# Performance work log

Hardware: AMD Instinct MI355X
Metric: run time of the kernel (lower is better)

The kernel has to match this reference:

```python
import jax, jax.numpy as jnp
import numpy as np

E, H, I = 5, 768, 1024  # num_experts, hidden_dim, intermediate_dim
TOP_K = 2


def setup_inputs() -> dict:
    key = jax.random.key(0)
    ks = jax.random.split(key, 6)
    s = 0.02
    return {
        "x": jax.random.normal(ks[0], (4, 2048, H), dtype=jnp.float32),
        "router_w": jax.random.normal(ks[1], (E, H), dtype=jnp.float32) * s,  # torch Linear (out,in)
        "router_b": jnp.zeros((E,), dtype=jnp.float32),
        "gate_w": jax.random.normal(ks[2], (E, H, I), dtype=jnp.float32) * s,
        "up_w": jax.random.normal(ks[3], (E, H, I), dtype=jnp.float32) * s,
        "down_w": jax.random.normal(ks[4], (E, I, H), dtype=jnp.float32) * s,
    }


def reference(x, router_w, router_b, gate_w, up_w, down_w):
    B, S, Hd = x.shape
    xf = x.reshape(-1, Hd)                       # [T, H]
    T = xf.shape[0]
    # Router: linear (with bias) -> softmax -> top-2 -> renormalize
    logits = xf @ router_w.T + router_b          # [T, E]
    scores = jax.nn.softmax(logits, axis=-1)
    vals, idx = jax.lax.top_k(scores, TOP_K)     # [T, 2]
    vals = vals / jnp.sum(vals, axis=-1, keepdims=True)
    # Dense combine weights: zero for unselected experts (same math as the
    # per-expert gather/scatter loop in the original module).
    comb = jnp.zeros((T, gate_w.shape[0]), dtype=x.dtype)
    comb = comb.at[jnp.arange(T)[:, None], idx].add(vals)  # [T, E]
    # SwiGLU per expert, vectorized over experts
    g = jnp.einsum('th,ehi->tei', xf, gate_w)    # [T, E, I]
    u = jnp.einsum('th,ehi->tei', xf, up_w)
    y = jnp.einsum('tei,eih->teh', jax.nn.silu(g) * u, down_w)  # [T, E, H]
    out = jnp.einsum('teh,te->th', y, comb)
    return out.reshape(B, S, Hd)
```

## Files before the change

### kernel.cpp

```cpp
#include <hip/hip_runtime.h>
#include <hip/hip_bf16.h>
#include <cstdint>
#include <cstddef>

#define T_TOK 8192
#define H_DIM 768
#define I_DIM 1024
#define N_EXP 5
#define MAXTILE 136

typedef short v8s __attribute__((ext_vector_type(8)));
typedef float v4f __attribute__((ext_vector_type(4)));

static __device__ __forceinline__ unsigned short f2bf(float f) {
    union { float f; unsigned int u; } v; v.f = f;
    unsigned int u = v.u;
    unsigned int r = (u + 0x7fffu + ((u >> 16) & 1u)) >> 16;
    return (unsigned short)r;
}
static __device__ __forceinline__ float bf2f(unsigned short s) {
    union { unsigned int u; float f; } v; v.u = ((unsigned int)s) << 16; return v.f;
}

static __device__ __forceinline__ void async16(const unsigned short* g, unsigned short* l) {
    __builtin_amdgcn_global_load_lds(
        (const __attribute__((address_space(1))) unsigned int*)g,
        (__attribute__((address_space(3))) unsigned int*)l, 16, 0, 0);
}

__global__ void k_prep(const float* __restrict__ gw, const float* __restrict__ uw,
                       const float* __restrict__ dw,
                       unsigned short* __restrict__ wbt, unsigned short* __restrict__ dbt,
                       const float* __restrict__ x, const float* __restrict__ rw,
                       const float* __restrict__ rb, unsigned short* __restrict__ xb,
                       int* __restrict__ top2e, float2* __restrict__ top2w) {
    const int z = blockIdx.z;
    const int tid = threadIdx.x;
    if (z < 3 * N_EXP) {
        __shared__ float tile[32][33];
        const int row = tid >> 3, cq = tid & 7;
        const int ocol = tid >> 3, seg = tid & 7;
        if (z < 2 * N_EXP) {
            if (blockIdx.y >= H_DIM / 32) return;
            const int e = z % N_EXP;
            const int isUp = z >= N_EXP;
            const float* src = (isUp ? uw : gw) + (size_t)e * H_DIM * I_DIM;
            const int c0 = blockIdx.x * 32, r0 = blockIdx.y * 32;
            float4 v = *(const float4*)(src + (size_t)(r0 + row) * I_DIM + c0 + cq * 4);
            tile[row][cq * 4 + 0] = v.x; tile[row][cq * 4 + 1] = v.y;
            tile[row][cq * 4 + 2] = v.z; tile[row][cq * 4 + 3] = v.w;
            __syncthreads();
            int c = c0 + ocol;
            int orow = (c >> 4) * 32 + (c & 15) + (isUp ? 16 : 0);
            ushort4 o;
            o.x = f2bf(tile[seg * 4 + 0][ocol]); o.y = f2bf(tile[seg * 4 + 1][ocol]);
            o.z = f2bf(tile[seg * 4 + 2][ocol]); o.w = f2bf(tile[seg * 4 + 3][ocol]);
            *(ushort4*)(wbt + ((size_t)e * 2 * I_DIM + orow) * H_DIM + r0 + seg * 4) = o;
        } else {
            if (blockIdx.x >= H_DIM / 32) return;
            const int e = z - 2 * N_EXP;
            const float* src = dw + (size_t)e * I_DIM * H_DIM;
            unsigned short* dst = dbt + (size_t)e * I_DIM * H_DIM;
            const int c0 = blockIdx.x * 32, r0 = blockIdx.y * 32;
            float4 v = *(const float4*)(src + (size_t)(r0 + row) * H_DIM + c0 + cq * 4);
            tile[row][cq * 4 + 0] = v.x; tile[row][cq * 4 + 1] = v.y;
            tile[row][cq * 4 + 2] = v.z; tile[row][cq * 4 + 3] = v.w;
            __syncthreads();
            ushort4 o;
            o.x = f2bf(tile[seg * 4 + 0][ocol]); o.y = f2bf(tile[seg * 4 + 1][ocol]);
            o.z = f2bf(tile[seg * 4 + 2][ocol]); o.w = f2bf(tile[seg * 4 + 3][ocol]);
            *(ushort4*)(dst + (size_t)(c0 + ocol) * I_DIM + r0 + seg * 4) = o;
        }
    } else {
        const int wave = tid >> 6, lane = tid & 63;
        const int t = (((z - 3 * N_EXP) * 1024 + blockIdx.y * 32 + blockIdx.x) * 4) + wave;
        const float* xr = x + (size_t)t * H_DIM;
        unsigned short* xbr = xb + (size_t)t * H_DIM;
        float acc[N_EXP];
#pragma unroll
        for (int e = 0; e < N_EXP; e++) acc[e] = 0.f;
#pragma unroll
        for (int j = 0; j < H_DIM / 256; j++) {
            int idx = j * 256 + lane * 4;
            float4 xv = *(const float4*)(xr + idx);
            ushort4 o;
            o.x = f2bf(xv.x); o.y = f2bf(xv.y); o.z = f2bf(xv.z); o.w = f2bf(xv.w);
            *(ushort4*)(xbr + idx) = o;
#pragma unroll
            for (int e = 0; e < N_EXP; e++) {
                float4 wv = *(const float4*)(rw + e * H_DIM + idx);
                acc[e] += xv.x * wv.x + xv.y * wv.y + xv.z * wv.z + xv.w * wv.w;
            }
        }
#pragma unroll
        for (int s = 32; s > 0; s >>= 1) {
#pragma unroll
            for (int e = 0; e < N_EXP; e++) acc[e] += __shfl_down(acc[e], s);
        }
        if (lane == 0) {
            float l[N_EXP];
#pragma unroll
            for (int e = 0; e < N_EXP; e++) l[e] = acc[e] + rb[e];
            int i1 = 0;
#pragma unroll
            for (int e = 1; e < N_EXP; e++) if (l[e] > l[i1]) i1 = e;
            int i2 = (i1 == 0) ? 1 : 0;
#pragma unroll
            for (int e = 0; e < N_EXP; e++) if (e != i1 && l[e] > l[i2]) i2 = e;
            float w1 = 1.f / (1.f + __expf(l[i2] - l[i1]));
            top2e[t] = i1 | (i2 << 8);
            top2w[t] = make_float2(w1, 1.f - w1);
        }
    }
}

__global__ void k_router_b(const int* __restrict__ top2e, const float2* __restrict__ top2w,
                           int* __restrict__ cnt, int* __restrict__ tokslot,
                           float* __restrict__ pweight, int* __restrict__ done,
                           int4* __restrict__ tiles) {
    __shared__ int lcnt[N_EXP], lbase[N_EXP];
    const int tid = threadIdx.x;
    if (tid < N_EXP) lcnt[tid] = 0;
    __syncthreads();
    const int t = blockIdx.x * 256 + tid;
    const int pe = top2e[t];
    const float2 wv = top2w[t];
    const int e1 = pe & 0xff, e2 = pe >> 8;
    const int s1 = atomicAdd(&lcnt[e1], 1);
    const int s2 = atomicAdd(&lcnt[e2], 1);
    __syncthreads();
    if (tid < N_EXP) lbase[tid] = atomicAdd(&cnt[tid], lcnt[tid]);
    __syncthreads();
    const int p1 = lbase[e1] + s1;
    tokslot[e1 * T_TOK + p1] = t; pweight[e1 * T_TOK + p1] = wv.x;
    const int p2 = lbase[e2] + s2;
    tokslot[e2 * T_TOK + p2] = t | (1 << 16); pweight[e2 * T_TOK + p2] = wv.y;
    __syncthreads();
    if (tid == 0) {
        __threadfence();
        if (atomicAdd(done, 1) == (int)gridDim.x - 1) {
            int c[N_EXP], off = 0, idx = 0;
            for (int e = 0; e < N_EXP; e++) c[e] = atomicAdd(&cnt[e], 0);
            for (int e = 0; e < N_EXP; e++) {
                for (int m0 = 0; m0 < c[e]; m0 += 128)
                    tiles[idx++] = make_int4(e, m0, off, c[e]);
                off += c[e];
            }
            for (; idx < MAXTILE; idx++) tiles[idx] = make_int4(-1, 0, 0, 0);
        }
    }
}

__launch_bounds__(256, 4)
__global__ void k_gateup(const unsigned short* __restrict__ xb,
                         const unsigned short* __restrict__ wbt,
                         const int4* __restrict__ tiles,
                         const int* __restrict__ tokslot,
                         const float* __restrict__ pweight,
                         unsigned short* __restrict__ hbuf) {
    const int4 td = tiles[blockIdx.x];
    const int e = td.x;
    if (e < 0) return;
    const int m0 = td.y, offe = td.z, cn = td.w;
    const int n0 = blockIdx.y * 64;

    __shared__ __align__(16) unsigned short ldsA[128 * 64];
    __shared__ __align__(16) unsigned short ldsB[128 * 64];
    __shared__ int tokLds[128];
    __shared__ float pwLds[128];

    const int tid = threadIdx.x;
    if (tid < 128) {
        int gr = m0 + tid;
        int tk = 0; float pw = 0.f;
        if (gr < cn) { tk = tokslot[e * T_TOK + gr] & 0xFFFF; pw = pweight[e * T_TOK + gr]; }
        tokLds[tid] = tk; pwLds[tid] = pw;
    }
    __syncthreads();

    const int lane = tid & 63;
    const int wave = tid >> 6;
    const int fm = lane & 15, quad = lane >> 4;

    const int prow = lane >> 3;
    const int pc = lane & 7;
    const int lc8 = (pc ^ prow) * 8;

    unsigned aOff[4];
#pragma unroll
    for (int c = 0; c < 4; c++)
        aOff[c] = (unsigned)tokLds[c * 32 + wave * 8 + prow] * H_DIM;
    const unsigned short* aBase = xb + lc8;
    const unsigned short* bBase =
        wbt + ((size_t)e * 2 * I_DIM + n0 * 2 + wave * 8 + prow) * H_DIM + lc8;
    unsigned short* ldsAW = ldsA + wave * 8 * 64;
    unsigned short* ldsBW = ldsB + wave * 8 * 64;

    const int wm = (wave & 1) * 64, wnw = wave >> 1;

    v4f acc[4][4];
#pragma unroll
    for (int i = 0; i < 4; i++)
#pragma unroll
        for (int j = 0; j < 4; j++) acc[i][j] = (v4f)0.f;

    for (int kb = 0; kb < H_DIM / 64; kb++) {
        const int k0 = kb * 64;
#pragma unroll
        for (int c = 0; c < 4; c++)
            async16(aBase + aOff[c] + k0, ldsAW + c * 32 * 64);
#pragma unroll
        for (int c = 0; c < 4; c++)
            async16(bBase + (size_t)c * 32 * H_DIM + k0, ldsBW + c * 32 * 64);
        __syncthreads();
#pragma unroll
        for (int ks = 0; ks < 2; ks++) {
            const int pq = ((ks * 4 + quad) ^ (fm & 7)) * 8;
            v8s aF[4], bF[4];
#pragma unroll
            for (int im = 0; im < 4; im++)
                aF[im] = *(const v8s*)&ldsA[(wm + im * 16 + fm) * 64 + pq];
#pragma unroll
            for (int in = 0; in < 4; in++)
                bF[in] = *(const v8s*)&ldsB[(wnw * 64 + in * 16 + fm) * 64 + pq];
#pragma unroll
            for (int im = 0; im < 4; im++)
#pragma unroll
                for (int in = 0; in < 4; in++)
                    acc[im][in] = __builtin_amdgcn_mfma_f32_16x16x32_bf16(aF[im], bF[in], acc[im][in], 0, 0, 0);
        }
        __syncthreads();
    }

#pragma unroll
    for (int im = 0; im < 4; im++) {
#pragma unroll
        for (int reg = 0; reg < 4; reg++) {
            int lr = wm + im * 16 + quad * 4 + reg;
            int gr = m0 + lr;
            if (gr < cn) {
                float pw = pwLds[lr];
                size_t base = (size_t)(offe + gr) * I_DIM + n0 + wnw * 32 + fm;
#pragma unroll
                for (int j = 0; j < 2; j++) {
                    float g = acc[im][2 * j][reg];
                    float u = acc[im][2 * j + 1][reg];
                    float s = g / (1.f + __expf(-g));
                    hbuf[base + j * 16] = f2bf(s * u * pw);
                }
            }
        }
    }
}

__launch_bounds__(256, 4)
__global__ void k_down(const unsigned short* __restrict__ hbuf,
                       const unsigned short* __restrict__ dbt,
                       const int4* __restrict__ tiles,
                       const int* __restrict__ tokslot,
                       unsigned short* __restrict__ ybuf) {
    const int4 td = tiles[blockIdx.x];
    const int e = td.x;
    if (e < 0) return;
    const int m0 = td.y, offe = td.z, cn = td.w;
    const int n0 = blockIdx.y * 128;

    __shared__ __align__(16) unsigned short ldsA[128 * 64];
    __shared__ __align__(16) unsigned short ldsB[128 * 64];
    __shared__ int tokLds[128];

    const int tid = threadIdx.x;
    if (tid < 128) {
        int gr = m0 + tid;
        tokLds[tid] = (gr < cn) ? tokslot[e * T_TOK + gr] : 0;
    }
    __syncthreads();

    const int lane = tid & 63;
    const int wave = tid >> 6;
    const int fm = lane & 15, quad = lane >> 4;

    const int prow = lane >> 3;
    const int pc = lane & 7;
    const int lc8 = (pc ^ prow) * 8;

    unsigned aOff[4];
#pragma unroll
    for (int c = 0; c < 4; c++) {
        int ar = m0 + c * 32 + wave * 8 + prow;
        if (ar >= cn) ar = cn - 1;
        aOff[c] = (unsigned)(offe + ar) * I_DIM;
    }
    const unsigned short* aBase = hbuf + lc8;
    const unsigned short* bBase =
        dbt + ((size_t)e * H_DIM + n0 + wave * 8 + prow) * I_DIM + lc8;
    unsigned short* ldsAW = ldsA + wave * 8 * 64;
    unsigned short* ldsBW = ldsB + wave * 8 * 64;

    const int wm = (wave & 1) * 64, wn = (wave >> 1) * 64;

    v4f acc[4][4];
#pragma unroll
    for (int i = 0; i < 4; i++)
#pragma unroll
        for (int j = 0; j < 4; j++) acc[i][j] = (v4f)0.f;

    for (int kb = 0; kb < I_DIM / 64; kb++) {
        const int k0 = kb * 64;
#pragma unroll
        for (int c = 0; c < 4; c++)
            async16(aBase + aOff[c] + k0, ldsAW + c * 32 * 64);
#pragma unroll
        for (int c = 0; c < 4; c++)
            async16(bBase + (size_t)c * 32 * I_DIM + k0, ldsBW + c * 32 * 64);
        __syncthreads();
#pragma unroll
        for (int ks = 0; ks < 2; ks++) {
            const int pq = ((ks * 4 + quad) ^ (fm & 7)) * 8;
            v8s aF[4], bF[4];
#pragma unroll
            for (int im = 0; im < 4; im++)
                aF[im] = *(const v8s*)&ldsA[(wm + im * 16 + fm) * 64 + pq];
#pragma unroll
            for (int in = 0; in < 4; in++)
                bF[in] = *(const v8s*)&ldsB[(wn + in * 16 + fm) * 64 + pq];
#pragma unroll
            for (int im = 0; im < 4; im++)
#pragma unroll
                for (int in = 0; in < 4; in++)
                    acc[im][in] = __builtin_amdgcn_mfma_f32_16x16x32_bf16(aF[im], bF[in], acc[im][in], 0, 0, 0);
        }
        __syncthreads();
    }

#pragma unroll
    for (int im = 0; im < 4; im++) {
#pragma unroll
        for (int reg = 0; reg < 4; reg++) {
            int lr = wm + im * 16 + quad * 4 + reg;
            int gr = m0 + lr;
            if (gr < cn) {
                int v = tokLds[lr];
                int tok = v & 0xFFFF, s = (v >> 16) & 1;
#pragma unroll
                for (int in = 0; in < 4; in++) {
                    int col = n0 + wn + in * 16 + fm;
                    ybuf[((size_t)s * T_TOK + tok) * H_DIM + col] = f2bf(acc[im][in][reg]);
                }
            }
        }
    }
}

__global__ void k_combine(const unsigned short* __restrict__ ybuf, float* __restrict__ out) {
    const size_t i8 = ((size_t)blockIdx.x * 256 + threadIdx.x) * 8;
    const unsigned short* y0 = ybuf + i8;
    const unsigned short* y1 = ybuf + (size_t)T_TOK * H_DIM + i8;
    ushort4 a0 = *(const ushort4*)y0, a1 = *(const ushort4*)(y0 + 4);
    ushort4 b0 = *(const ushort4*)y1, b1 = *(const ushort4*)(y1 + 4);
    float4 o0, o1;
    o0.x = bf2f(a0.x) + bf2f(b0.x); o0.y = bf2f(a0.y) + bf2f(b0.y);
    o0.z = bf2f(a0.z) + bf2f(b0.z); o0.w = bf2f(a0.w) + bf2f(b0.w);
    o1.x = bf2f(a1.x) + bf2f(b1.x); o1.y = bf2f(a1.y) + bf2f(b1.y);
    o1.z = bf2f(a1.z) + bf2f(b1.z); o1.w = bf2f(a1.w) + bf2f(b1.w);
    *(float4*)(out + i8) = o0;
    *(float4*)(out + i8 + 4) = o1;
}

extern "C" void kernel_launch(void* const* d_in, const int* in_sizes, int n_in,
                              void* d_out, int out_size, void* d_ws, size_t ws_size,
                              hipStream_t stream) {
    const float* x  = (const float*)d_in[0];
    const float* rw = (const float*)d_in[1];
    const float* rb = (const float*)d_in[2];
    const float* gw = (const float*)d_in[3];
    const float* uw = (const float*)d_in[4];
    const float* dw = (const float*)d_in[5];
    float* out = (float*)d_out;

    char* ws = (char*)d_ws;
    size_t o = 0;
    auto alloc = [&](size_t bytes) { void* p = ws + o; o += (bytes + 255) & ~255ull; return p; };
    int*    cnt     = (int*)   alloc(8 * 4);
    int*    tokslot = (int*)   alloc((size_t)N_EXP * T_TOK * 4);
    float*  pweight = (float*) alloc((size_t)N_EXP * T_TOK * 4);
    int*    top2e   = (int*)   alloc((size_t)T_TOK * 4);
    float2* top2w   = (float2*)alloc((size_t)T_TOK * 8);
    int4*   tiles   = (int4*)  alloc((size_t)MAXTILE * 16);
    unsigned short* xb   = (unsigned short*)alloc((size_t)T_TOK * H_DIM * 2);
    unsigned short* wbt  = (unsigned short*)alloc((size_t)N_EXP * 2 * I_DIM * H_DIM * 2);
    unsigned short* dbt  = (unsigned short*)alloc((size_t)N_EXP * H_DIM * I_DIM * 2);
    unsigned short* hbuf = (unsigned short*)alloc((size_t)(2 * T_TOK + 128) * I_DIM * 2);
    unsigned short* ybuf = (unsigned short*)alloc((size_t)2 * T_TOK * H_DIM * 2);

    hipMemsetAsync(cnt, 0, 8 * 4, stream);

    dim3 pg(I_DIM / 32, I_DIM / 32, 3 * N_EXP + 2);
    k_prep<<<pg, 256, 0, stream>>>(gw, uw, dw, wbt, dbt, x, rw, rb, xb, top2e, top2w);

    k_router_b<<<T_TOK / 256, 256, 0, stream>>>(top2e, top2w, cnt, tokslot, pweight,
                                                cnt + 5, tiles);

    dim3 g1(MAXTILE, I_DIM / 64);
    k_gateup<<<g1, 256, 0, stream>>>(xb, wbt, tiles, tokslot, pweight, hbuf);

    dim3 g2(MAXTILE, H_DIM / 128);
    k_down<<<g2, 256, 0, stream>>>(hbuf, dbt, tiles, tokslot, ybuf);

    k_combine<<<(T_TOK * H_DIM) / (256 * 8), 256, 0, stream>>>(ybuf, out);
}
```

Baseline: 232.9 us.

## Rewrite gate/up GEMM as 256x256 tile with double-buffered ping-pong pipeline

The gate/up expert GEMM now uses 512-thread blocks covering 256 tokens by 256 interleaved gate/up columns, with its own 256-row tile list built in the router kernel. The K loop is restructured into a double-buffered LDS pipeline where async global-to-LDS loads for later k-steps are issued between MFMA phases, gated by explicit vmcnt waits, barriers and s_setprio. The goal is to hide load latency and raise data reuse per block. In exchange it uses far more LDS and registers per block, lowers occupancy, and leaves more padded work in each expert's last partial tile.

```diff
diff --git a/kernel.cpp b/kernel.cpp
--- a/kernel.cpp
+++ b/kernel.cpp
@@ -8,6 +8,7 @@
 #define I_DIM 1024
 #define N_EXP 5
 #define MAXTILE 136
+#define MAXT2 72
 
 typedef short v8s __attribute__((ext_vector_type(8)));
 typedef float v4f __attribute__((ext_vector_type(4)));
@@ -117,7 +118,7 @@
 __global__ void k_router_b(const int* __restrict__ top2e, const float2* __restrict__ top2w,
                            int* __restrict__ cnt, int* __restrict__ tokslot,
                            float* __restrict__ pweight, int* __restrict__ done,
-                           int4* __restrict__ tiles) {
+                           int4* __restrict__ tiles, int4* __restrict__ tiles2) {
     __shared__ int lcnt[N_EXP], lbase[N_EXP];
     const int tid = threadIdx.x;
     if (tid < N_EXP) lcnt[tid] = 0;
@@ -147,30 +148,37 @@
                 off += c[e];
             }
             for (; idx < MAXTILE; idx++) tiles[idx] = make_int4(-1, 0, 0, 0);
-        }
-    }
-}
-
-__launch_bounds__(256, 4)
+            int off2 = 0, idx2 = 0;
+            for (int e = 0; e < N_EXP; e++) {
+                for (int m0 = 0; m0 < c[e]; m0 += 256)
+                    tiles2[idx2++] = make_int4(e, m0, off2, c[e]);
+                off2 += c[e];
+            }
+            for (; idx2 < MAXT2; idx2++) tiles2[idx2] = make_int4(-1, 0, 0, 0);
+        }
+    }
+}
+
+__launch_bounds__(512, 2)
 __global__ void k_gateup(const unsigned short* __restrict__ xb,
                          const unsigned short* __restrict__ wbt,
-                         const int4* __restrict__ tiles,
+                         const int4* __restrict__ tiles2,
                          const int* __restrict__ tokslot,
                          const float* __restrict__ pweight,
                          unsigned short* __restrict__ hbuf) {
-    const int4 td = tiles[blockIdx.x];
+    const int4 td = tiles2[blockIdx.y];
     const int e = td.x;
     if (e < 0) return;
     const int m0 = td.y, offe = td.z, cn = td.w;
-    const int n0 = blockIdx.y * 64;
-
-    __shared__ __align__(16) unsigned short ldsA[128 * 64];
-    __shared__ __align__(16) unsigned short ldsB[128 * 64];
-    __shared__ int tokLds[128];
-    __shared__ float pwLds[128];
+    const int by = blockIdx.x;
+
+    __shared__ __align__(16) unsigned short ldsA[2][256 * 64];
+    __shared__ __align__(16) unsigned short ldsB[2][256 * 64];
+    __shared__ int tokLds[256];
+    __shared__ float pwLds[256];
 
     const int tid = threadIdx.x;
-    if (tid < 128) {
+    if (tid < 256) {
         int gr = m0 + tid;
         int tk = 0; float pw = 0.f;
         if (gr < cn) { tk = tokslot[e * T_TOK + gr] & 0xFFFF; pw = pweight[e * T_TOK + gr]; }
@@ -179,68 +187,161 @@
     __syncthreads();
 
     const int lane = tid & 63;
-    const int wave = tid >> 6;
+    const int w = tid >> 6;
     const int fm = lane & 15, quad = lane >> 4;
+    const int wm = (w >> 2) * 128;
+    const int wn = w & 3;
 
     const int prow = lane >> 3;
     const int pc = lane & 7;
     const int lc8 = (pc ^ prow) * 8;
 
-    unsigned aOff[4];
-#pragma unroll
-    for (int c = 0; c < 4; c++)
-        aOff[c] = (unsigned)tokLds[c * 32 + wave * 8 + prow] * H_DIM;
+    unsigned aOff[2][2];
+#pragma unroll
+    for (int h = 0; h < 2; h++)
+#pragma unroll
+        for (int c = 0; c < 2; c++)
+            aOff[h][c] = (unsigned)tokLds[h * 128 + w * 16 + c * 8 + prow] * H_DIM;
     const unsigned short* aBase = xb + lc8;
     const unsigned short* bBase =
-        wbt + ((size_t)e * 2 * I_DIM + n0 * 2 + wave * 8 + prow) * H_DIM + lc8;
-    unsigned short* ldsAW = ldsA + wave * 8 * 64;
-    unsigned short* ldsBW = ldsB + wave * 8 * 64;
-
-    const int wm = (wave & 1) * 64, wnw = wave >> 1;
-
-    v4f acc[4][4];
-#pragma unroll
-    for (int i = 0; i < 4; i++)
+        wbt + ((size_t)e * 2 * I_DIM + by * 256 + w * 16 + prow) * H_DIM + lc8;
+
+#define STAGE_A(buf, h, kt) do { \
+        async16(aBase + aOff[h][0] + (kt) * 64, &ldsA[buf][((h) * 128 + w * 16 + 0) * 64]); \
+        async16(aBase + aOff[h][1] + (kt) * 64, &ldsA[buf][((h) * 128 + w * 16 + 8) * 64]); \
+    } while (0)
+#define STAGE_B(buf, h, kt) do { \
+        async16(bBase + (size_t)((h) * 128 + 0) * H_DIM + (kt) * 64, &ldsB[buf][((h) * 128 + w * 16 + 0) * 64]); \
+        async16(bBase + (size_t)((h) * 128 + 8) * H_DIM + (kt) * 64, &ldsB[buf][((h) * 128 + w * 16 + 8) * 64]); \
+    } while (0)
+
+    v4f acc[8][4];
+#pragma unroll
+    for (int i = 0; i < 8; i++)
 #pragma unroll
         for (int j = 0; j < 4; j++) acc[i][j] = (v4f)0.f;
 
-    for (int kb = 0; kb < H_DIM / 64; kb++) {
-        const int k0 = kb * 64;
-#pragma unroll
-        for (int c = 0; c < 4; c++)
-            async16(aBase + aOff[c] + k0, ldsAW + c * 32 * 64);
-#pragma unroll
-        for (int c = 0; c < 4; c++)
-            async16(bBase + (size_t)c * 32 * H_DIM + k0, ldsBW + c * 32 * 64);
-        __syncthreads();
-#pragma unroll
-        for (int ks = 0; ks < 2; ks++) {
-            const int pq = ((ks * 4 + quad) ^ (fm & 7)) * 8;
-            v8s aF[4], bF[4];
-#pragma unroll
-            for (int im = 0; im < 4; im++)
-                aF[im] = *(const v8s*)&ldsA[(wm + im * 16 + fm) * 64 + pq];
-#pragma unroll
-            for (int in = 0; in < 4; in++)
-                bF[in] = *(const v8s*)&ldsB[(wnw * 64 + in * 16 + fm) * 64 + pq];
-#pragma unroll
-            for (int im = 0; im < 4; im++)
-#pragma unroll
-                for (int in = 0; in < 4; in++)
-                    acc[im][in] = __builtin_amdgcn_mfma_f32_16x16x32_bf16(aF[im], bF[in], acc[im][in], 0, 0, 0);
-        }
-        __syncthreads();
-    }
-
-#pragma unroll
-    for (int im = 0; im < 4; im++) {
+    STAGE_A(0, 0, 0); STAGE_A(0, 1, 0); STAGE_B(0, 0, 0); STAGE_B(0, 1, 0);
+    STAGE_A(1, 0, 1); STAGE_A(1, 1, 1); STAGE_B(1, 0, 1);
+    __builtin_amdgcn_sched_barrier(0);
+    asm volatile("s_waitcnt vmcnt(6)" ::: "memory");
+    __builtin_amdgcn_s_barrier();
+    __builtin_amdgcn_sched_barrier(0);
+
+#pragma unroll 2
+    for (int t = 0; t < H_DIM / 64; t++) {
+        const int cur = t & 1;
+        const unsigned short* A = ldsA[cur];
+        const unsigned short* Bm = ldsB[cur];
+        v8s a03[4][2], a47[4][2], b01[2][2], b23[2][2];
+
+#pragma unroll
+        for (int im = 0; im < 4; im++)
+#pragma unroll
+            for (int ks = 0; ks < 2; ks++)
+                a03[im][ks] = *(const v8s*)&A[(wm + im * 16 + fm) * 64 + (((ks * 4 + quad) ^ (fm & 7)) * 8)];
+#pragma unroll
+        for (int in = 0; in < 2; in++)
+#pragma unroll
+            for (int ks = 0; ks < 2; ks++)
+                b01[in][ks] = *(const v8s*)&Bm[(wn * 64 + in * 16 + fm) * 64 + (((ks * 4 + quad) ^ (fm & 7)) * 8)];
+        if (t + 1 < H_DIM / 64) STAGE_B(cur ^ 1, 1, t + 1);
+        __builtin_amdgcn_sched_barrier(0);
+        __builtin_amdgcn_s_barrier();
+        __builtin_amdgcn_sched_barrier(0);
+        __builtin_amdgcn_s_setprio(1);
+#pragma unroll
+        for (int im = 0; im < 4; im++)
+#pragma unroll
+            for (int in = 0; in < 2; in++)
+#pragma unroll
+                for (int ks = 0; ks < 2; ks++)
+                    acc[im][in] = __builtin_amdgcn_mfma_f32_16x16x32_bf16(a03[im][ks], b01[in][ks], acc[im][in], 0, 0, 0);
+        __builtin_amdgcn_s_setprio(0);
+        __builtin_amdgcn_sched_barrier(0);
+        __builtin_amdgcn_s_barrier();
+        __builtin_amdgcn_sched_barrier(0);
+
+#pragma unroll
+        for (int im = 0; im < 4; im++)
+#pragma unroll
+            for (int ks = 0; ks < 2; ks++)
+                a47[im][ks] = *(const v8s*)&A[(wm + (im + 4) * 16 + fm) * 64 + (((ks * 4 + quad) ^ (fm & 7)) * 8)];
+        __builtin_amdgcn_sched_barrier(0);
+        __builtin_amdgcn_s_barrier();
+        __builtin_amdgcn_sched_barrier(0);
+        __builtin_amdgcn_s_setprio(1);
+#pragma unroll
+        for (int im = 0; im < 4; im++)
+#pragma unroll
+            for (int in = 0; in < 2; in++)
+#pragma unroll
+                for (int ks = 0; ks < 2; ks++)
+                    acc[im + 4][in] = __builtin_amdgcn_mfma_f32_16x16x32_bf16(a47[im][ks], b01[in][ks], acc[im + 4][in], 0, 0, 0);
+        __builtin_amdgcn_s_setprio(0);
+        __builtin_amdgcn_sched_barrier(0);
+        __builtin_amdgcn_s_barrier();
+        __builtin_amdgcn_sched_barrier(0);
+
+#pragma unroll
+        for (int in = 0; in < 2; in++)
+#pragma unroll
+            for (int ks = 0; ks < 2; ks++)
+                b23[in][ks] = *(const v8s*)&Bm[(wn * 64 + (in + 2) * 16 + fm) * 64 + (((ks * 4 + quad) ^ (fm & 7)) * 8)];
+        if (t + 2 < H_DIM / 64) { STAGE_A(cur, 0, t + 2); STAGE_A(cur, 1, t + 2); }
+        __builtin_amdgcn_sched_barrier(0);
+        __builtin_amdgcn_s_barrier();
+        __builtin_amdgcn_sched_barrier(0);
+        __builtin_amdgcn_s_setprio(1);
+#pragma unroll
+        for (int im = 0; im < 4; im++)
+#pragma unroll
+            for (int in = 0; in < 2; in++)
+#pragma unroll
+                for (int ks = 0; ks < 2; ks++)
+                    acc[im][in + 2] = __builtin_amdgcn_mfma_f32_16x16x32_bf16(a03[im][ks], b23[in][ks], acc[im][in + 2], 0, 0, 0);
+        __builtin_amdgcn_s_setprio(0);
+        __builtin_amdgcn_sched_barrier(0);
+        __builtin_amdgcn_s_barrier();
+        __builtin_amdgcn_sched_barrier(0);
+
+        if (t + 2 < H_DIM / 64) STAGE_B(cur, 0, t + 2);
+        __builtin_amdgcn_sched_barrier(0);
+        __builtin_amdgcn_s_barrier();
+        __builtin_amdgcn_sched_barrier(0);
+        __builtin_amdgcn_s_setprio(1);
+#pragma unroll
+        for (int im = 0; im < 4; im++)
+#pragma unroll
+            for (int in = 0; in < 2; in++)
+#pragma unroll
+                for (int ks = 0; ks < 2; ks++)
+                    acc[im + 4][in + 2] = __builtin_amdgcn_mfma_f32_16x16x32_bf16(a47[im][ks], b23[in][ks], acc[im + 4][in + 2], 0, 0, 0);
+        __builtin_amdgcn_s_setprio(0);
+        __builtin_amdgcn_sched_barrier(0);
+
+        if (t < H_DIM / 64 - 2) {
+            asm volatile("s_waitcnt vmcnt(6)" ::: "memory");
+            __builtin_amdgcn_s_barrier();
+            __builtin_amdgcn_sched_barrier(0);
+        } else if (t == H_DIM / 64 - 2) {
+            asm volatile("s_waitcnt vmcnt(0)" ::: "memory");
+            __builtin_amdgcn_s_barrier();
+            __builtin_amdgcn_sched_barrier(0);
+        }
+    }
+#undef STAGE_A
+#undef STAGE_B
+
+#pragma unroll
+    for (int im = 0; im < 8; im++) {
 #pragma unroll
         for (int reg = 0; reg < 4; reg++) {
             int lr = wm + im * 16 + quad * 4 + reg;
             int gr = m0 + lr;
             if (gr < cn) {
                 float pw = pwLds[lr];
-                size_t base = (size_t)(offe + gr) * I_DIM + n0 + wnw * 32 + fm;
+                size_t base = (size_t)(offe + gr) * I_DIM + by * 128 + wn * 32 + fm;
 #pragma unroll
                 for (int j = 0; j < 2; j++) {
                     float g = acc[im][2 * j][reg];
@@ -387,10 +488,11 @@
     int*    top2e   = (int*)   alloc((size_t)T_TOK * 4);
     float2* top2w   = (float2*)alloc((size_t)T_TOK * 8);
     int4*   tiles   = (int4*)  alloc((size_t)MAXTILE * 16);
+    int4*   tiles2  = (int4*)  alloc((size_t)MAXT2 * 16);
     unsigned short* xb   = (unsigned short*)alloc((size_t)T_TOK * H_DIM * 2);
     unsigned short* wbt  = (unsigned short*)alloc((size_t)N_EXP * 2 * I_DIM * H_DIM * 2);
     unsigned short* dbt  = (unsigned short*)alloc((size_t)N_EXP * H_DIM * I_DIM * 2);
-    unsigned short* hbuf = (unsigned short*)alloc((size_t)(2 * T_TOK + 128) * I_DIM * 2);
+    unsigned short* hbuf = (unsigned short*)alloc((size_t)(2 * T_TOK + 256) * I_DIM * 2);
     unsigned short* ybuf = (unsigned short*)alloc((size_t)2 * T_TOK * H_DIM * 2);
 
     hipMemsetAsync(cnt, 0, 8 * 4, stream);
@@ -399,10 +501,10 @@
     k_prep<<<pg, 256, 0, stream>>>(gw, uw, dw, wbt, dbt, x, rw, rb, xb, top2e, top2w);
 
     k_router_b<<<T_TOK / 256, 256, 0, stream>>>(top2e, top2w, cnt, tokslot, pweight,
-                                                cnt + 5, tiles);
-
-    dim3 g1(MAXTILE, I_DIM / 64);
-    k_gateup<<<g1, 256, 0, stream>>>(xb, wbt, tiles, tokslot, pweight, hbuf);
+                                                cnt + 5, tiles, tiles2);
+
+    dim3 g1(I_DIM / 128, MAXT2);
+    k_gateup<<<g1, 512, 0, stream>>>(xb, wbt, tiles2, tokslot, pweight, hbuf);
 
     dim3 g2(MAXTILE, H_DIM / 128);
     k_down<<<g2, 256, 0, stream>>>(hbuf, dbt, tiles, tokslot, ybuf);
```

Result: slower. 257.4 us (+10.5%).
